# Optimization experiments

Measured on AMD Instinct MI355X. Metric: run time of the kernel, lower is better.

Reference implementation:

```python
import jax, jax.numpy as jnp
import numpy as np

NUM_HEAD = 16


def setup_inputs() -> dict:
    key = jax.random.key(0)
    k1, k2, k3 = jax.random.split(key, 3)
    E = 1024
    x = jax.random.normal(k1, (4, 2048, E), dtype=jnp.float32)
    W1 = jax.random.normal(k2, (E, 3 * E), dtype=jnp.float32) * 0.02
    b1 = jnp.zeros((3 * E,), dtype=jnp.float32)
    W2 = jax.random.normal(k3, (E, E), dtype=jnp.float32) * 0.02
    b2 = jnp.zeros((E,), dtype=jnp.float32)
    return {"x": x, "W1": W1, "b1": b1, "W2": W2, "b2": b2}


def reference(x, W1, b1, W2, b2):
    # Fused QKV projection: (n, s, 3E)
    h = x @ W1 + b1
    n, s, _ = h.shape
    # Split into heads FIRST (matches torch reshape), then transpose: (n, H, s, 3*d_head)
    h = h.reshape(n, s, NUM_HEAD, -1).transpose(0, 2, 1, 3)
    # Chunk last dim into q, k, v: each (n, H, s, d_head)
    q, k, v = jnp.split(h, 3, axis=-1)
    dk = jnp.asarray(v.shape[-1], x.dtype) ** 0.5
    # Naive full S x S attention (faithful to source)
    w = jnp.einsum("nhqd,nhkd->nhqk", q, k) / dk
    w = jax.nn.softmax(w, axis=-1)  # dropout1 is identity at eval
    att = jnp.einsum("nhqk,nhkd->nhqd", w, v)
    att = att.transpose(0, 2, 1, 3).reshape(n, s, -1)  # (n, s, E)
    return att @ W2 + b2  # dropout2 identity at eval
```

## Files before the change

### kernel.cpp

```cpp
#include <hip/hip_runtime.h>
#include <math.h>
#include <stdint.h>
#include <stddef.h>


#define SEQ    2048
#define NB     4
#define E_DIM  1024
#define N1     3072
#define M_TOK  8192
#define NHEAD  16
#define DHEAD  64

typedef __attribute__((ext_vector_type(4))) float    floatx4;
typedef __attribute__((ext_vector_type(8))) short    shortx8;
typedef __attribute__((ext_vector_type(4))) short    shortx4;
typedef __attribute__((ext_vector_type(4))) unsigned short ushortx4;

#if __has_builtin(__builtin_amdgcn_exp2f)
#define EXP2(x) __builtin_amdgcn_exp2f(x)
#else
#define EXP2(x) __expf((x) * 0.6931471805599453f)
#endif

#define MFMA_K16(a, b, c) \
    __builtin_amdgcn_mfma_f32_16x16x16bf16_1k((a), (b), (c), 0, 0, 0)

__device__ __forceinline__ unsigned short f2bf(float f) {
    union { float f; unsigned u; } v; v.f = f;
    unsigned r = (v.u + 0x7FFFu + ((v.u >> 16) & 1u)) >> 16;
    return (unsigned short)r;
}
__device__ __forceinline__ unsigned fbits(float f) {
    union { float f; unsigned u; } v; v.f = f; return v.u;
}

__device__ __forceinline__ void gl_lds16(const void* g, void* l) {
    __builtin_amdgcn_global_load_lds(
        (const __attribute__((address_space(1))) unsigned int*)g,
        (__attribute__((address_space(3))) unsigned int*)l, 16, 0, 0);
}

__global__ __launch_bounds__(256) void cvt_bf16(
    const float* __restrict__ in, unsigned short* __restrict__ out)
{
    const size_t i = ((size_t)blockIdx.x * 256 + threadIdx.x) * 8;
    float4 a = *(const float4*)(in + i);
    float4 b = *(const float4*)(in + i + 4);
    ushortx4 o0 = { f2bf(a.x), f2bf(a.y), f2bf(a.z), f2bf(a.w) };
    ushortx4 o1 = { f2bf(b.x), f2bf(b.y), f2bf(b.z), f2bf(b.w) };
    *(ushortx4*)(out + i)     = o0;
    *(ushortx4*)(out + i + 4) = o1;
}

__global__ __launch_bounds__(256) void cvt_transpose(
    const float* __restrict__ W, unsigned short* __restrict__ Wt, int K, int N)
{
    __shared__ unsigned short tile[32][33];
    const int tx = threadIdx.x, ty = threadIdx.y;
    const int n0 = blockIdx.x * 32, k0 = blockIdx.y * 32;
#pragma unroll
    for (int r = 0; r < 4; ++r) {
        const int k = ty + r * 8;
        tile[tx][k] = f2bf(W[(size_t)(k0 + k) * N + n0 + tx]);
    }
    __syncthreads();
#pragma unroll
    for (int r = 0; r < 4; ++r) {
        const int n = ty + r * 8;
        Wt[(size_t)(n0 + n) * K + k0 + tx] = tile[n][tx];
    }
}

template <bool OUT_BF16, bool FUSE>
__global__ __launch_bounds__(256) void gemm_bf16(
    const short* __restrict__ A, const short* __restrict__ Bt,
    const float* __restrict__ bias, void* __restrict__ Cout,
    unsigned short* __restrict__ Vt,
    int M, int N, int K)
{
    __shared__ short As[128 * 64];
    __shared__ short Bs[128 * 64];

    const int t    = threadIdx.x;
    const int lane = t & 63, w = t >> 6;
    const int quad = lane >> 4, l15 = lane & 15;
    const int bm = blockIdx.y * 128, bn = blockIdx.x * 128;
    const int m0w = (w >> 1) * 64, n0w = (w & 1) * 64;

    const int srow   = t >> 3;
    const int schunk = t & 7;
    const int gch    = schunk ^ (srow & 7);
    const short* Ag = A  + (size_t)(bm + srow) * K + gch * 8;
    const short* Bg = Bt + (size_t)(bn + srow) * K + gch * 8;
    short* Al = As + srow * 64 + schunk * 8;
    short* Bl = Bs + srow * 64 + schunk * 8;

    floatx4 acc[4][4];
#pragma unroll
    for (int i = 0; i < 4; ++i)
#pragma unroll
        for (int j = 0; j < 4; ++j) acc[i][j] = (floatx4)0.f;

    for (int k0 = 0; k0 < K; k0 += 64) {
        __syncthreads();
#pragma unroll
        for (int r = 0; r < 4; ++r) {
            gl_lds16(Ag + (size_t)(r * 32) * K + k0, Al + r * 32 * 64);
            gl_lds16(Bg + (size_t)(r * 32) * K + k0, Bl + r * 32 * 64);
        }
        __syncthreads();

#pragma unroll
        for (int kk = 0; kk < 2; ++kk) {
            shortx8 af[4], bf[4];
#pragma unroll
            for (int mi = 0; mi < 4; ++mi)
                af[mi] = *(const shortx8*)(As + (m0w + mi * 16 + l15) * 64
                                           + (((kk * 4 + quad) ^ (l15 & 7)) * 8));
#pragma unroll
            for (int ni = 0; ni < 4; ++ni)
                bf[ni] = *(const shortx8*)(Bs + (n0w + ni * 16 + l15) * 64
                                           + (((kk * 4 + quad) ^ (l15 & 7)) * 8));
#pragma unroll
            for (int mi = 0; mi < 4; ++mi)
#pragma unroll
                for (int ni = 0; ni < 4; ++ni)
                    acc[mi][ni] = __builtin_amdgcn_mfma_f32_16x16x32_bf16(
                        af[mi], bf[ni], acc[mi][ni], 0, 0, 0);
        }
    }

    float bv[4];
#pragma unroll
    for (int ni = 0; ni < 4; ++ni) bv[ni] = bias[bn + n0w + ni * 16 + l15];

#pragma unroll
    for (int ni = 0; ni < 4; ++ni) {
        const int col   = bn + n0w + ni * 16 + l15;
        const int cm    = col % 192;
        const int vhead = col / 192;
#pragma unroll
        for (int mi = 0; mi < 4; ++mi) {
            const int row0 = bm + m0w + mi * 16 + quad * 4;
            float v[4];
#pragma unroll
            for (int r = 0; r < 4; ++r) v[r] = acc[mi][ni][r] + bv[ni];
            if (OUT_BF16) {
                if (FUSE && cm < DHEAD) {
#pragma unroll
                    for (int r = 0; r < 4; ++r) v[r] *= 0.18033688011112042f;
                }
                unsigned short* H = (unsigned short*)Cout;
#pragma unroll
                for (int r = 0; r < 4; ++r)
                    H[(size_t)(row0 + r) * N + col] = f2bf(v[r]);
                if (FUSE && cm >= 2 * DHEAD) {
                    const int nb = row0 >> 11;
                    const int s  = row0 & 2047;
                    const int d  = cm - 2 * DHEAD;
                    ushortx4 pk = { f2bf(v[0]), f2bf(v[1]), f2bf(v[2]), f2bf(v[3]) };
                    *(ushortx4*)(Vt + ((size_t)(nb * NHEAD + vhead) * DHEAD + d) * SEQ + s) = pk;
                }
            } else {
                float* C = (float*)Cout;
#pragma unroll
                for (int r = 0; r < 4; ++r)
                    C[(size_t)(row0 + r) * N + col] = v[r];
            }
        }
    }
}

__global__ __launch_bounds__(256, 4) void attn_mfma(
    const short* __restrict__ h, const short* __restrict__ Vt,
    unsigned short* __restrict__ att)
{
    __shared__ short Ks[2][64 * 64];
    __shared__ short Vs[2][64 * 64];

    const int t    = threadIdx.x;
    const int lane = t & 63, w = t >> 6;
    const int quad = lane >> 4, l15 = lane & 15;
    const int r7   = l15 & 7;
    const int bh = blockIdx.x, n = bh >> 4, head = bh & 15;
    const int q0 = blockIdx.y * 128 + w * 32;

    const short* hQ  = h + (size_t)n * SEQ * N1 + head * (3 * DHEAD);
    const short* hK  = hQ + DHEAD;
    const short* Vtb = Vt + (size_t)bh * DHEAD * SEQ;

    const int srow = t >> 2;
    const int sc0  = (t & 3) * 2;
    const int sk   = srow & 7;
    const short* gK = hK  + (size_t)srow * N1  + sc0 * 8;
    const short* gV = Vtb + (size_t)srow * SEQ + sc0 * 8;
    const int oL0 = srow * 64 + ((sc0    ) ^ sk) * 8;
    const int oL1 = srow * 64 + ((sc0 + 1) ^ sk) * 8;

    shortx8 qf[2][2];
#pragma unroll
    for (int qt = 0; qt < 2; ++qt)
#pragma unroll
        for (int kt = 0; kt < 2; ++kt)
            qf[qt][kt] = *(const shortx8*)(hQ + (size_t)(q0 + qt * 16 + l15) * N1
                                           + kt * 32 + quad * 8);

    floatx4 O[2][4];
    float lsum[2] = { 0.f, 0.f };
#pragma unroll
    for (int qt = 0; qt < 2; ++qt)
#pragma unroll
        for (int dt = 0; dt < 4; ++dt) O[qt][dt] = (floatx4)0.f;

    const int NT = SEQ / 64;

    int4 ka = *(const int4*)gK, kb = *(const int4*)(gK + 8);
    int4 va = *(const int4*)gV, vb = *(const int4*)(gV + 8);
    *(int4*)(&Ks[0][oL0]) = ka; *(int4*)(&Ks[0][oL1]) = kb;
    *(int4*)(&Vs[0][oL0]) = va; *(int4*)(&Vs[0][oL1]) = vb;
    gK += (size_t)64 * N1; gV += 64;

    for (int it = 0; it < NT; ++it) {
        const int buf = it & 1;
        __syncthreads();

        const bool more = (it + 1 < NT);
        if (more) {
            ka = *(const int4*)gK; kb = *(const int4*)(gK + 8);
            va = *(const int4*)gV; vb = *(const int4*)(gV + 8);
            gK += (size_t)64 * N1; gV += 64;
        }

        const short* Kb = &Ks[buf][0];
        const short* Vb = &Vs[buf][0];

        __builtin_amdgcn_s_setprio(1);
#pragma unroll
        for (int sl = 0; sl < 4; ++sl) {
            const short* krow = Kb + (sl * 16 + l15) * 64;
            shortx8 kf0 = *(const shortx8*)(krow + ((quad ^ r7) * 8));
            shortx8 kf1 = *(const shortx8*)(krow + (((quad ^ 4) ^ r7) * 8));
            shortx4 vf[4];
#pragma unroll
            for (int dt = 0; dt < 4; ++dt)
                vf[dt] = *(const shortx4*)(Vb + (dt * 16 + l15) * 64
                                           + (((sl * 4 + quad) ^ (r7 << 1)) << 2));

            shortx4 pa[2];
#pragma unroll
            for (int qt = 0; qt < 2; ++qt) {
                floatx4 s = __builtin_amdgcn_mfma_f32_16x16x32_bf16(
                    kf0, qf[qt][0], (floatx4)0.f, 0, 0, 0);
                s = __builtin_amdgcn_mfma_f32_16x16x32_bf16(
                    kf1, qf[qt][1], s, 0, 0, 0);
                const float p0 = EXP2(s[0]);
                const float p1 = EXP2(s[1]);
                const float p2 = EXP2(s[2]);
                const float p3 = EXP2(s[3]);
                lsum[qt] += (p0 + p1) + (p2 + p3);
                union { uint2 u; shortx4 v; } cv;
                cv.u.x = __builtin_amdgcn_perm(fbits(p1), fbits(p0), 0x07060302u);
                cv.u.y = __builtin_amdgcn_perm(fbits(p3), fbits(p2), 0x07060302u);
                pa[qt] = cv.v;
            }

#pragma unroll
            for (int qt = 0; qt < 2; ++qt)
#pragma unroll
                for (int dt = 0; dt < 4; ++dt)
                    O[qt][dt] = MFMA_K16(pa[qt], vf[dt], O[qt][dt]);
        }
        __builtin_amdgcn_s_setprio(0);

        if (more) {
            short* Kn = &Ks[buf ^ 1][0];
            short* Vn = &Vs[buf ^ 1][0];
            *(int4*)(Kn + oL0) = ka; *(int4*)(Kn + oL1) = kb;
            *(int4*)(Vn + oL0) = va; *(int4*)(Vn + oL1) = vb;
        }
    }

#pragma unroll
    for (int qt = 0; qt < 2; ++qt) {
        lsum[qt] += __shfl_xor(lsum[qt], 16);
        lsum[qt] += __shfl_xor(lsum[qt], 32);
    }

    const size_t obase = ((size_t)n * SEQ + q0) * E_DIM + head * DHEAD;
#pragma unroll
    for (int qt = 0; qt < 2; ++qt)
#pragma unroll
        for (int r = 0; r < 4; ++r) {
            const float inv = 1.f / __shfl(lsum[qt], quad * 4 + r);
            const size_t row = obase + (size_t)(qt * 16 + quad * 4 + r) * E_DIM;
#pragma unroll
            for (int dt = 0; dt < 4; ++dt)
                att[row + dt * 16 + l15] = f2bf(O[qt][dt][r] * inv);
        }
}

extern "C" void kernel_launch(void* const* d_in, const int* in_sizes, int n_in,
                              void* d_out, int out_size, void* d_ws, size_t ws_size,
                              hipStream_t stream)
{
    const float* x  = (const float*)d_in[0];
    const float* W1 = (const float*)d_in[1];
    const float* b1 = (const float*)d_in[2];
    const float* W2 = (const float*)d_in[3];
    const float* b2 = (const float*)d_in[4];
    float* out = (float*)d_out;

    char* ws = (char*)d_ws;
    unsigned short* x_bf  = (unsigned short*)(ws);
    unsigned short* W1t   = (unsigned short*)(ws + (16u << 20));
    unsigned short* W2t   = (unsigned short*)(ws + (22u << 20));
    unsigned short* h_bf  = (unsigned short*)(ws + (24u << 20));
    unsigned short* attb  = (unsigned short*)(ws + (72u << 20));
    unsigned short* Vtw   = (unsigned short*)(ws + (88u << 20));

    cvt_bf16<<<dim3((M_TOK * E_DIM) / (256 * 8)), 256, 0, stream>>>(x, x_bf);
    cvt_transpose<<<dim3(N1 / 32, E_DIM / 32), dim3(32, 8), 0, stream>>>(W1, W1t, E_DIM, N1);
    cvt_transpose<<<dim3(E_DIM / 32, E_DIM / 32), dim3(32, 8), 0, stream>>>(W2, W2t, E_DIM, E_DIM);

    gemm_bf16<true, true><<<dim3(N1 / 128, M_TOK / 128), 256, 0, stream>>>(
        (const short*)x_bf, (const short*)W1t, b1, h_bf, Vtw, M_TOK, N1, E_DIM);

    attn_mfma<<<dim3(NB * NHEAD, SEQ / 128), 256, 0, stream>>>(
        (const short*)h_bf, (const short*)Vtw, attb);

    gemm_bf16<false, false><<<dim3(E_DIM / 128, M_TOK / 128), 256, 0, stream>>>(
        (const short*)attb, (const short*)W2t, b2, out, nullptr, M_TOK, E_DIM, E_DIM);
}
```

Before: 277.9 us.

## Load attention K/V tiles directly into LDS and hoist fragment reads

```diff
diff --git a/kernel.cpp b/kernel.cpp
--- a/kernel.cpp
+++ b/kernel.cpp
@@ -172,7 +172,7 @@
     }
 }
 
-__global__ __launch_bounds__(256, 4) void attn_mfma(
+__global__ __launch_bounds__(256, 2) void attn_mfma(
     const short* __restrict__ h, const short* __restrict__ Vt,
     unsigned short* __restrict__ att)
 {
@@ -190,13 +190,10 @@
     const short* hK  = hQ + DHEAD;
     const short* Vtb = Vt + (size_t)bh * DHEAD * SEQ;
 
-    const int srow = t >> 2;
-    const int sc0  = (t & 3) * 2;
-    const int sk   = srow & 7;
-    const short* gK = hK  + (size_t)srow * N1  + sc0 * 8;
-    const short* gV = Vtb + (size_t)srow * SEQ + sc0 * 8;
-    const int oL0 = srow * 64 + ((sc0    ) ^ sk) * 8;
-    const int oL1 = srow * 64 + ((sc0 + 1) ^ sk) * 8;
+    const int srow = t >> 3, schunk = t & 7;
+    const int gch  = schunk ^ (srow & 7);
+    const short* gKs = hK  + (size_t)srow * N1  + gch * 8;
+    const short* gVs = Vtb + (size_t)srow * SEQ + gch * 8;
 
     shortx8 qf[2][2];
 #pragma unroll
@@ -215,45 +212,55 @@
 
     const int NT = SEQ / 64;
 
-    int4 ka = *(const int4*)gK, kb = *(const int4*)(gK + 8);
-    int4 va = *(const int4*)gV, vb = *(const int4*)(gV + 8);
-    *(int4*)(&Ks[0][oL0]) = ka; *(int4*)(&Ks[0][oL1]) = kb;
-    *(int4*)(&Vs[0][oL0]) = va; *(int4*)(&Vs[0][oL1]) = vb;
-    gK += (size_t)64 * N1; gV += 64;
+    {
+        short* Kd = (short*)Ks[0] + t * 8;
+        short* Vd = (short*)Vs[0] + t * 8;
+        gl_lds16(gKs, Kd);
+        gl_lds16(gKs + (size_t)32 * N1, Kd + 2048);
+        gl_lds16(gVs, Vd);
+        gl_lds16(gVs + 32 * SEQ, Vd + 2048);
+    }
 
     for (int it = 0; it < NT; ++it) {
         const int buf = it & 1;
         __syncthreads();
 
-        const bool more = (it + 1 < NT);
-        if (more) {
-            ka = *(const int4*)gK; kb = *(const int4*)(gK + 8);
-            va = *(const int4*)gV; vb = *(const int4*)(gV + 8);
-            gK += (size_t)64 * N1; gV += 64;
+        if (it + 1 < NT) {
+            const int kv = (it + 1) * 64;
+            short* Kd = (short*)Ks[buf ^ 1] + t * 8;
+            short* Vd = (short*)Vs[buf ^ 1] + t * 8;
+            gl_lds16(gKs + (size_t)kv * N1, Kd);
+            gl_lds16(gKs + (size_t)(kv + 32) * N1, Kd + 2048);
+            gl_lds16(gVs + kv, Vd);
+            gl_lds16(gVs + kv + 32 * SEQ, Vd + 2048);
         }
 
         const short* Kb = &Ks[buf][0];
         const short* Vb = &Vs[buf][0];
 
-        __builtin_amdgcn_s_setprio(1);
+        shortx8 kfr[4][2];
+        shortx4 vfr[4][4];
 #pragma unroll
         for (int sl = 0; sl < 4; ++sl) {
             const short* krow = Kb + (sl * 16 + l15) * 64;
-            shortx8 kf0 = *(const shortx8*)(krow + ((quad ^ r7) * 8));
-            shortx8 kf1 = *(const shortx8*)(krow + (((quad ^ 4) ^ r7) * 8));
-            shortx4 vf[4];
+            kfr[sl][0] = *(const shortx8*)(krow + ((quad ^ r7) * 8));
+            kfr[sl][1] = *(const shortx8*)(krow + (((quad ^ 4) ^ r7) * 8));
 #pragma unroll
             for (int dt = 0; dt < 4; ++dt)
-                vf[dt] = *(const shortx4*)(Vb + (dt * 16 + l15) * 64
-                                           + (((sl * 4 + quad) ^ (r7 << 1)) << 2));
-
+                vfr[sl][dt] = *(const shortx4*)(Vb + (dt * 16 + l15) * 64
+                                                + (((sl * 4 + quad) ^ (r7 << 1)) << 2));
+        }
+
+        __builtin_amdgcn_s_setprio(1);
+#pragma unroll
+        for (int sl = 0; sl < 4; ++sl) {
             shortx4 pa[2];
 #pragma unroll
             for (int qt = 0; qt < 2; ++qt) {
                 floatx4 s = __builtin_amdgcn_mfma_f32_16x16x32_bf16(
-                    kf0, qf[qt][0], (floatx4)0.f, 0, 0, 0);
+                    kfr[sl][0], qf[qt][0], (floatx4)0.f, 0, 0, 0);
                 s = __builtin_amdgcn_mfma_f32_16x16x32_bf16(
-                    kf1, qf[qt][1], s, 0, 0, 0);
+                    kfr[sl][1], qf[qt][1], s, 0, 0, 0);
                 const float p0 = EXP2(s[0]);
                 const float p1 = EXP2(s[1]);
                 const float p2 = EXP2(s[2]);
@@ -269,16 +276,9 @@
             for (int qt = 0; qt < 2; ++qt)
 #pragma unroll
                 for (int dt = 0; dt < 4; ++dt)
-                    O[qt][dt] = MFMA_K16(pa[qt], vf[dt], O[qt][dt]);
+                    O[qt][dt] = MFMA_K16(pa[qt], vfr[sl][dt], O[qt][dt]);
         }
         __builtin_amdgcn_s_setprio(0);
-
-        if (more) {
-            short* Kn = &Ks[buf ^ 1][0];
-            short* Vn = &Vs[buf ^ 1][0];
-            *(int4*)(Kn + oL0) = ka; *(int4*)(Kn + oL1) = kb;
-            *(int4*)(Vn + oL0) = va; *(int4*)(Vn + oL1) = vb;
-        }
     }
 
 #pragma unroll
```

Result: slower. 294.2 us (+5.8%).

## Shrink attention query tile to 16 rows per wave and single-buffer K/V

Applied to the files above, without the earlier changes.

```diff
diff --git a/kernel.cpp b/kernel.cpp
--- a/kernel.cpp
+++ b/kernel.cpp
@@ -176,15 +176,15 @@
     const short* __restrict__ h, const short* __restrict__ Vt,
     unsigned short* __restrict__ att)
 {
-    __shared__ short Ks[2][64 * 64];
-    __shared__ short Vs[2][64 * 64];
+    __shared__ short Ks[64 * 64];
+    __shared__ short Vs[64 * 64];
 
     const int t    = threadIdx.x;
     const int lane = t & 63, w = t >> 6;
     const int quad = lane >> 4, l15 = lane & 15;
     const int r7   = l15 & 7;
     const int bh = blockIdx.x, n = bh >> 4, head = bh & 15;
-    const int q0 = blockIdx.y * 128 + w * 32;
+    const int q0 = blockIdx.y * 64 + w * 16;
 
     const short* hQ  = h + (size_t)n * SEQ * N1 + head * (3 * DHEAD);
     const short* hK  = hQ + DHEAD;
@@ -198,106 +198,83 @@
     const int oL0 = srow * 64 + ((sc0    ) ^ sk) * 8;
     const int oL1 = srow * 64 + ((sc0 + 1) ^ sk) * 8;
 
-    shortx8 qf[2][2];
-#pragma unroll
-    for (int qt = 0; qt < 2; ++qt)
-#pragma unroll
-        for (int kt = 0; kt < 2; ++kt)
-            qf[qt][kt] = *(const shortx8*)(hQ + (size_t)(q0 + qt * 16 + l15) * N1
-                                           + kt * 32 + quad * 8);
-
-    floatx4 O[2][4];
-    float lsum[2] = { 0.f, 0.f };
-#pragma unroll
-    for (int qt = 0; qt < 2; ++qt)
-#pragma unroll
-        for (int dt = 0; dt < 4; ++dt) O[qt][dt] = (floatx4)0.f;
+    shortx8 qf[2];
+#pragma unroll
+    for (int kt = 0; kt < 2; ++kt)
+        qf[kt] = *(const shortx8*)(hQ + (size_t)(q0 + l15) * N1 + kt * 32 + quad * 8);
+
+    floatx4 O[4];
+    float lsum = 0.f;
+#pragma unroll
+    for (int dt = 0; dt < 4; ++dt) O[dt] = (floatx4)0.f;
 
     const int NT = SEQ / 64;
 
     int4 ka = *(const int4*)gK, kb = *(const int4*)(gK + 8);
     int4 va = *(const int4*)gV, vb = *(const int4*)(gV + 8);
-    *(int4*)(&Ks[0][oL0]) = ka; *(int4*)(&Ks[0][oL1]) = kb;
-    *(int4*)(&Vs[0][oL0]) = va; *(int4*)(&Vs[0][oL1]) = vb;
     gK += (size_t)64 * N1; gV += 64;
 
     for (int it = 0; it < NT; ++it) {
-        const int buf = it & 1;
         __syncthreads();
-
-        const bool more = (it + 1 < NT);
-        if (more) {
-            ka = *(const int4*)gK; kb = *(const int4*)(gK + 8);
-            va = *(const int4*)gV; vb = *(const int4*)(gV + 8);
+        *(int4*)(Ks + oL0) = ka;
+        *(int4*)(Ks + oL1) = kb;
+        *(int4*)(Vs + oL0) = va;
+        *(int4*)(Vs + oL1) = vb;
+        __syncthreads();
+
+        if (it + 1 < NT) {
+            ka = *(const int4*)gK;
+            kb = *(const int4*)(gK + 8);
+            va = *(const int4*)gV;
+            vb = *(const int4*)(gV + 8);
             gK += (size_t)64 * N1; gV += 64;
         }
 
-        const short* Kb = &Ks[buf][0];
-        const short* Vb = &Vs[buf][0];
-
         __builtin_amdgcn_s_setprio(1);
 #pragma unroll
         for (int sl = 0; sl < 4; ++sl) {
-            const short* krow = Kb + (sl * 16 + l15) * 64;
+            const short* krow = Ks + (sl * 16 + l15) * 64;
             shortx8 kf0 = *(const shortx8*)(krow + ((quad ^ r7) * 8));
             shortx8 kf1 = *(const shortx8*)(krow + (((quad ^ 4) ^ r7) * 8));
             shortx4 vf[4];
 #pragma unroll
             for (int dt = 0; dt < 4; ++dt)
-                vf[dt] = *(const shortx4*)(Vb + (dt * 16 + l15) * 64
+                vf[dt] = *(const shortx4*)(Vs + (dt * 16 + l15) * 64
                                            + (((sl * 4 + quad) ^ (r7 << 1)) << 2));
 
-            shortx4 pa[2];
-#pragma unroll
-            for (int qt = 0; qt < 2; ++qt) {
-                floatx4 s = __builtin_amdgcn_mfma_f32_16x16x32_bf16(
-                    kf0, qf[qt][0], (floatx4)0.f, 0, 0, 0);
-                s = __builtin_amdgcn_mfma_f32_16x16x32_bf16(
-                    kf1, qf[qt][1], s, 0, 0, 0);
-                const float p0 = EXP2(s[0]);
-                const float p1 = EXP2(s[1]);
-                const float p2 = EXP2(s[2]);
-                const float p3 = EXP2(s[3]);
-                lsum[qt] += (p0 + p1) + (p2 + p3);
-                union { uint2 u; shortx4 v; } cv;
-                cv.u.x = __builtin_amdgcn_perm(fbits(p1), fbits(p0), 0x07060302u);
-                cv.u.y = __builtin_amdgcn_perm(fbits(p3), fbits(p2), 0x07060302u);
-                pa[qt] = cv.v;
-            }
-
-#pragma unroll
-            for (int qt = 0; qt < 2; ++qt)
-#pragma unroll
-                for (int dt = 0; dt < 4; ++dt)
-                    O[qt][dt] = MFMA_K16(pa[qt], vf[dt], O[qt][dt]);
+            floatx4 s = __builtin_amdgcn_mfma_f32_16x16x32_bf16(
+                kf0, qf[0], (floatx4)0.f, 0, 0, 0);
+            s = __builtin_amdgcn_mfma_f32_16x16x32_bf16(
+                kf1, qf[1], s, 0, 0, 0);
+            const float p0 = EXP2(s[0]);
+            const float p1 = EXP2(s[1]);
+            const float p2 = EXP2(s[2]);
+            const float p3 = EXP2(s[3]);
+            lsum += (p0 + p1) + (p2 + p3);
+            union { uint2 u; shortx4 v; } cv;
+            cv.u.x = __builtin_amdgcn_perm(fbits(p1), fbits(p0), 0x07060302u);
+            cv.u.y = __builtin_amdgcn_perm(fbits(p3), fbits(p2), 0x07060302u);
+            const shortx4 pa = cv.v;
+
+#pragma unroll
+            for (int dt = 0; dt < 4; ++dt)
+                O[dt] = MFMA_K16(pa, vf[dt], O[dt]);
         }
         __builtin_amdgcn_s_setprio(0);
-
-        if (more) {
-            short* Kn = &Ks[buf ^ 1][0];
-            short* Vn = &Vs[buf ^ 1][0];
-            *(int4*)(Kn + oL0) = ka; *(int4*)(Kn + oL1) = kb;
-            *(int4*)(Vn + oL0) = va; *(int4*)(Vn + oL1) = vb;
-        }
-    }
-
-#pragma unroll
-    for (int qt = 0; qt < 2; ++qt) {
-        lsum[qt] += __shfl_xor(lsum[qt], 16);
-        lsum[qt] += __shfl_xor(lsum[qt], 32);
-    }
+    }
+
+    lsum += __shfl_xor(lsum, 16);
+    lsum += __shfl_xor(lsum, 32);
 
     const size_t obase = ((size_t)n * SEQ + q0) * E_DIM + head * DHEAD;
 #pragma unroll
-    for (int qt = 0; qt < 2; ++qt)
-#pragma unroll
-        for (int r = 0; r < 4; ++r) {
-            const float inv = 1.f / __shfl(lsum[qt], quad * 4 + r);
-            const size_t row = obase + (size_t)(qt * 16 + quad * 4 + r) * E_DIM;
-#pragma unroll
-            for (int dt = 0; dt < 4; ++dt)
-                att[row + dt * 16 + l15] = f2bf(O[qt][dt][r] * inv);
-        }
+    for (int r = 0; r < 4; ++r) {
+        const float inv = 1.f / __shfl(lsum, quad * 4 + r);
+        const size_t row = obase + (size_t)(quad * 4 + r) * E_DIM;
+#pragma unroll
+        for (int dt = 0; dt < 4; ++dt)
+            att[row + dt * 16 + l15] = f2bf(O[dt][r] * inv);
+    }
 }
 
 extern "C" void kernel_launch(void* const* d_in, const int* in_sizes, int n_in,
@@ -326,7 +303,7 @@
     gemm_bf16<true, true><<<dim3(N1 / 128, M_TOK / 128), 256, 0, stream>>>(
         (const short*)x_bf, (const short*)W1t, b1, h_bf, Vtw, M_TOK, N1, E_DIM);
 
-    attn_mfma<<<dim3(NB * NHEAD, SEQ / 128), 256, 0, stream>>>(
+    attn_mfma<<<dim3(NB * NHEAD, SEQ / 64), 256, 0, stream>>>(
         (const short*)h_bf, (const short*)Vtw, attb);
 
     gemm_bf16<false, false><<<dim3(E_DIM / 128, M_TOK / 128), 256, 0, stream>>>(
```

Measured after the change: 300.2 us. 1.08x slower.
